# Kernel optimization log

Measured on AMD Instinct MI355X. Metric: run time of the kernel, lower is better.

Reference implementation:

```python
import jax, jax.numpy as jnp
from jax import lax
import numpy as np


def _conv(x, w):
    # x: [B,Cin,H,W], w: [Cout,Cin,kh,kw] -> [B,Cout,H,W], SAME padding
    return lax.conv_general_dilated(x, w, (1, 1), 'SAME')


def setup_inputs() -> dict:
    key = jax.random.key(0)
    ks = jax.random.split(key, 16)
    B, Hh, W = 8, 256, 256
    inputs = jax.random.normal(ks[0], (B, Hh, W), jnp.float32)
    H0 = jax.random.normal(ks[1], (B, Hh, W), jnp.float32)
    C0 = jax.random.normal(ks[2], (B, 2, Hh, W), jnp.float32)
    # learned scalars: c2 ~ U(0,1), sf ~ N(0, 0.01) shifted away from 0 (it is a divisor)
    c2 = jax.random.uniform(ks[3], (1,), jnp.float32, 0.0, 1.0)
    sf = 0.01 * jax.random.normal(ks[4], (1,), jnp.float32) + 0.02
    # RedNet (assumed small conv encoder-decoder): 1->32->64->32->1, 3x3 SAME, ReLU
    w1 = 0.1 * jax.random.normal(ks[5], (32, 1, 3, 3), jnp.float32)
    b1 = jnp.zeros((32,), jnp.float32)
    w2 = 0.1 * jax.random.normal(ks[6], (64, 32, 3, 3), jnp.float32)
    b2 = jnp.zeros((64,), jnp.float32)
    w3 = 0.1 * jax.random.normal(ks[7], (32, 64, 3, 3), jnp.float32)
    b3 = jnp.zeros((32,), jnp.float32)
    w4 = 0.1 * jax.random.normal(ks[8], (1, 32, 3, 3), jnp.float32)
    b4 = jnp.zeros((1,), jnp.float32)
    return dict(inputs=inputs, H0=H0, C0=C0, c2=c2, sf=sf,
                w1=w1, b1=b1, w2=w2, b2=b2, w3=w3, b3=b3, w4=w4, b4=b4)


def reference(inputs, H0, C0, c2, sf, w1, b1, w2, b2, w3, b3, w4, b4):
    # Fixed 5-point Laplacian stencil (non-trainable in the original module)
    lap_k = jnp.array([[0., 1., 0.], [1., -4., 1.], [0., 1., 0.]],
                      dtype=inputs.dtype)[None, None]  # [1,1,3,3]

    # torch chain: C' = permute/matmul(Wcc^T)/permute + wcu*U
    #   reduces exactly to: C'[:,0] = inputs, C'[:,1] = C_old[:,0]
    C_new = jnp.stack([inputs, C0[:, 0]], axis=1)  # [B,2,H,W]

    V = inputs - H0  # [B,H,W]

    # H = whc . C' = 2*C'[:,0] - C'[:,1] = 2*inputs - C_old[:,0]
    lap = _conv(inputs[:, None], lap_k)[:, 0]  # [B,H,W]
    H = 2.0 * inputs - C0[:, 0] + c2 * lap

    # RedNet on scaled residual V
    h = (V / sf)[:, None]  # [B,1,H,W]
    h = jax.nn.relu(_conv(h, w1) + b1[None, :, None, None])
    h = jax.nn.relu(_conv(h, w2) + b2[None, :, None, None])
    h = jax.nn.relu(_conv(h, w3) + b3[None, :, None, None])
    V_hat = (_conv(h, w4) + b4[None, :, None, None])[:, 0] * sf  # [B,H,W]

    outputs = H + V_hat
    return (outputs, H, C_new, V, V_hat)
```

## Files before the change

kernel.cpp:

```cpp
#include <hip/hip_runtime.h>

#define PLANE 65536
#define WIDTH 256
#define PADW 258
#define PADPLANE 66564

typedef __bf16 v8bf __attribute__((ext_vector_type(8)));
typedef float  v4f  __attribute__((ext_vector_type(4)));

typedef const __attribute__((address_space(1))) unsigned int* gas_ptr;
typedef __attribute__((address_space(3))) unsigned int* las_ptr;

__device__ __forceinline__ void gl_lds(const void* g, void* l) {
  __builtin_amdgcn_global_load_lds((gas_ptr)g, (las_ptr)l, 16, 0, 0);
}

__device__ __forceinline__ int swz(int c) {
  return (c & ~7) | ((c & 7) ^ ((c >> 3) & 7));
}

__device__ __forceinline__ unsigned int pack2(float a, float b) {
  __bf16 ba = (__bf16)a, bb = (__bf16)b;
  unsigned short sa = __builtin_bit_cast(unsigned short, ba);
  unsigned short sb = __builtin_bit_cast(unsigned short, bb);
  return (unsigned int)sa | ((unsigned int)sb << 16);
}

#define WT_N 37440
#define ZR_N (8 * 1028 * 64)
__global__ __launch_bounds__(256) void wz_k(
    const float* __restrict__ w1, const float* __restrict__ w2,
    const float* __restrict__ w3, const float* __restrict__ w4,
    float* __restrict__ w1t, __bf16* __restrict__ B2t,
    __bf16* __restrict__ B3t, float* __restrict__ w4t,
    __bf16* __restrict__ a1, __bf16* __restrict__ a2,
    __bf16* __restrict__ a3)
{
  int t = blockIdx.x * 256 + threadIdx.x;
  if (t < WT_N) {
    if (t < 288) {
      int tap = t >> 5, cout = t & 31;
      w1t[t] = w1[cout * 9 + tap];
    }
    int t2 = t - 288;
    if (t2 >= 0 && t2 < 18432) {
      int cout = t2 / 288, k = t2 % 288;
      int tap = k / 32, cin = k % 32;
      B2t[t2] = (__bf16)w2[cout * 288 + cin * 9 + tap];
    }
    int t3 = t - (288 + 18432);
    if (t3 >= 0 && t3 < 18432) {
      int cout = t3 / 576, k = t3 % 576;
      int tap = k / 64, cin = k % 64;
      B3t[t3] = (__bf16)w3[cout * 576 + cin * 9 + tap];
    }
    int t4 = t - (288 + 18432 + 18432);
    if (t4 >= 0 && t4 < 288) {
      int tap = t4 >> 5, cin = t4 & 31;
      w4t[t4] = w4[cin * 9 + tap];
    }
    return;
  }
  int idx = t - WT_N;
  if (idx >= ZR_N) return;
  unsigned int* p; int C2;
  const int R1 = 8 * 1028 * 16, R2 = 8 * 1028 * 32;
  if (idx < R1)           { p = (unsigned int*)a1; C2 = 16; }
  else if (idx < R1 + R2) { p = (unsigned int*)a2; C2 = 32; idx -= R1; }
  else                    { p = (unsigned int*)a3; C2 = 16; idx -= R1 + R2; }
  int ch = idx % C2;
  int pr = idx / C2;
  int b = pr / 1028, r = pr % 1028;
  int y, x;
  if      (r < 258) { y = 0;           x = r; }
  else if (r < 516) { y = 257;         x = r - 258; }
  else if (r < 772) { y = r - 516 + 1; x = 0; }
  else              { y = r - 772 + 1; x = 257; }
  p[((size_t)b * PADPLANE + y * PADW + x) * C2 + ch] = 0;
}

__global__ __launch_bounds__(256) void prepconv1_k(
    const float* __restrict__ inputs, const float* __restrict__ H0,
    const float* __restrict__ C0, const float* __restrict__ c2p,
    const float* __restrict__ sfp, const float* __restrict__ w1t,
    const float* __restrict__ b1, float* __restrict__ dout,
    __bf16* __restrict__ act1)
{
  const int x = threadIdx.x, y = blockIdx.x, b = blockIdx.y;
  const int p = b * PLANE + y * WIDTH + x;
  const float c2 = c2p[0], sf = sfp[0], rsf = 1.0f / sf;

  float iv[3][3], hv[3][3];
  #pragma unroll
  for (int dy = 0; dy < 3; dy++) {
    int yy = y + dy - 1;
    #pragma unroll
    for (int dx = 0; dx < 3; dx++) {
      int xx = x + dx - 1;
      bool ok = (yy >= 0 && yy < 256 && xx >= 0 && xx < 256);
      int pn = p + (dy - 1) * WIDTH + (dx - 1);
      iv[dy][dx] = ok ? inputs[pn] : 0.f;
      hv[dy][dx] = ok ? H0[pn]     : 0.f;
    }
  }
  const float in = iv[1][1], h0 = hv[1][1];
  const float c0a = C0[b * 131072 + y * WIDTH + x];
  float lap = iv[0][1] + iv[2][1] + iv[1][0] + iv[1][2] - 4.f * in;
  float Hv = 2.f * in - c0a + c2 * lap;
  float V  = in - h0;
  dout[524288 + p]  = Hv;
  dout[2097152 + p] = V;
  dout[1048576 + b * 131072 + y * WIDTH + x]         = in;
  dout[1048576 + b * 131072 + 65536 + y * WIDTH + x] = c0a;

  float acc[32];
  #pragma unroll
  for (int i = 0; i < 32; i++) acc[i] = b1[i];
  #pragma unroll
  for (int tap = 0; tap < 9; tap++) {
    float v = (iv[tap / 3][tap % 3] - hv[tap / 3][tap % 3]) * rsf;
    const float* wp = w1t + tap * 32;
    #pragma unroll
    for (int i = 0; i < 32; i++) acc[i] = fmaf(wp[i], v, acc[i]);
  }
  unsigned int u[16];
  #pragma unroll
  for (int j = 0; j < 16; j++)
    u[j] = pack2(fmaxf(acc[2*j], 0.f), fmaxf(acc[2*j+1], 0.f));
  size_t pa = ((size_t)b * PADPLANE + (y+1) * PADW + (x+1)) * 32;
  uint4* op = reinterpret_cast<uint4*>(act1 + pa);
  #pragma unroll
  for (int j = 0; j < 4; j++)
    op[j] = make_uint4(u[4*j], u[4*j+1], u[4*j+2], u[4*j+3]);
}

#define C2ROWB 8320
template<int ROWS>
__global__ __launch_bounds__(256, 2) void conv2_k(
    const __bf16* __restrict__ in, const __bf16* __restrict__ Bt,
    const float* __restrict__ bias, __bf16* __restrict__ out)
{
  const int lane = threadIdx.x & 63, wave = threadIdx.x >> 6;
  const int l15 = lane & 15, q = lane >> 4;
  const int y0 = blockIdx.x * ROWS, xt = blockIdx.y, b = blockIdx.z;
  const int x0 = xt * 128;
  __shared__ __align__(16) char smem[3 * C2ROWB];
  const __bf16* plane = in + (size_t)b * PADPLANE * 32;

  auto stage = [&](int pr, char* lrow) {
    const char* g = (const char*)(plane + ((size_t)pr * PADW + x0) * 32);
    const int base = wave * 130;
    #pragma unroll
    for (int j = 0; j < 2; j++) {
      int c = base + j * 64 + lane;
      gl_lds(g + (size_t)swz(c) * 16, lrow + (base + j * 64) * 16);
    }
    if (lane < 2) {
      int c = base + 128 + lane;
      gl_lds(g + (size_t)swz(c) * 16, lrow + (base + 128) * 16);
    }
  };

  v8bf breg[9][4];
  #pragma unroll
  for (int tap = 0; tap < 9; tap++)
    #pragma unroll
    for (int nt = 0; nt < 4; nt++)
      breg[tap][nt] = *(const v8bf*)(Bt + (size_t)(nt * 16 + l15) * 288
                                        + tap * 32 + q * 8);
  float bv[4];
  #pragma unroll
  for (int nt = 0; nt < 4; nt++) bv[nt] = bias[nt * 16 + l15];

  #pragma unroll
  for (int r = 0; r < 3; r++) stage(y0 + r, smem + r * C2ROWB);
  __syncthreads();

  for (int i = 0; i < ROWS; i++) {
    v4f acc[2][4];
    #pragma unroll
    for (int mt = 0; mt < 2; mt++)
      #pragma unroll
      for (int nt = 0; nt < 4; nt++)
        acc[mt][nt] = (v4f){bv[nt], bv[nt], bv[nt], bv[nt]};

    #pragma unroll
    for (int tap = 0; tap < 9; tap++) {
      const int dy = tap / 3, dx = tap % 3;
      const char* srow = smem + ((i + dy) % 3) * C2ROWB;
      v8bf af[2];
      #pragma unroll
      for (int mt = 0; mt < 2; mt++) {
        int P = wave * 32 + mt * 16 + l15 + dx;
        af[mt] = *(const v8bf*)(srow + (size_t)swz(P * 4 + q) * 16);
      }
      #pragma unroll
      for (int mt = 0; mt < 2; mt++)
        #pragma unroll
        for (int nt = 0; nt < 4; nt++)
          acc[mt][nt] = __builtin_amdgcn_mfma_f32_16x16x32_bf16(
              af[mt], breg[tap][nt], acc[mt][nt], 0, 0, 0);
    }
    {
      size_t rb = ((size_t)b * PADPLANE + (size_t)(y0 + i + 1) * PADW
                   + x0 + 1) * 64;
      #pragma unroll
      for (int mt = 0; mt < 2; mt++) {
        #pragma unroll
        for (int r = 0; r < 4; r++) {
          size_t pa = rb + (size_t)(wave * 32 + mt * 16 + q * 4 + r) * 64;
          #pragma unroll
          for (int nt = 0; nt < 4; nt++)
            out[pa + nt * 16 + l15] = (__bf16)fmaxf(acc[mt][nt][r], 0.f);
        }
      }
    }
    __syncthreads();
    if (i + 3 < ROWS + 2)
      stage(y0 + i + 3, smem + (i % 3) * C2ROWB);
    __syncthreads();
  }
}

#define C3ROWB 16640
template<int ROWS>
__global__ __launch_bounds__(256, 2) void conv3_k(
    const __bf16* __restrict__ in, const __bf16* __restrict__ Bt,
    const float* __restrict__ bias, __bf16* __restrict__ out)
{
  const int lane = threadIdx.x & 63, wave = threadIdx.x >> 6;
  const int l15 = lane & 15, q = lane >> 4;
  const int y0 = blockIdx.x * ROWS, xt = blockIdx.y, b = blockIdx.z;
  const int x0 = xt * 128;
  __shared__ __align__(16) char smem[4 * C3ROWB];
  const __bf16* plane = in + (size_t)b * PADPLANE * 64;

  auto stage = [&](int pr, char* lrow) {
    const char* g = (const char*)(plane + ((size_t)pr * PADW + x0) * 64);
    const int base = wave * 260;
    #pragma unroll
    for (int j = 0; j < 4; j++) {
      int c = base + j * 64 + lane;
      gl_lds(g + (size_t)swz(c) * 16, lrow + (base + j * 64) * 16);
    }
    if (lane < 4) {
      int c = base + 256 + lane;
      gl_lds(g + (size_t)swz(c) * 16, lrow + (base + 256) * 16);
    }
  };

  v8bf breg[9][2][2];
  #pragma unroll
  for (int tap = 0; tap < 9; tap++)
    #pragma unroll
    for (int kb = 0; kb < 2; kb++)
      #pragma unroll
      for (int nt = 0; nt < 2; nt++)
        breg[tap][kb][nt] = *(const v8bf*)(Bt + (size_t)(nt * 16 + l15) * 576
                                              + tap * 64 + kb * 32 + q * 8);
  float bv[2] = {bias[l15], bias[16 + l15]};

  #pragma unroll
  for (int r = 0; r < 4; r++) stage(y0 + r, smem + r * C3ROWB);
  __syncthreads();

  for (int ps = 0; ps < ROWS / 2; ps++) {
    v4f acc[2][2][2];
    #pragma unroll
    for (int rr = 0; rr < 2; rr++)
      #pragma unroll
      for (int mt = 0; mt < 2; mt++)
        #pragma unroll
        for (int nt = 0; nt < 2; nt++)
          acc[rr][mt][nt] = (v4f){bv[nt], bv[nt], bv[nt], bv[nt]};

    #pragma unroll
    for (int t = 0; t < 4; t++) {
      const char* srow = smem + ((2 * ps + t) & 3) * C3ROWB;
      #pragma unroll
      for (int dx = 0; dx < 3; dx++) {
        #pragma unroll
        for (int kb = 0; kb < 2; kb++) {
          v8bf af[2];
          #pragma unroll
          for (int mt = 0; mt < 2; mt++) {
            int P = wave * 32 + mt * 16 + l15 + dx;
            af[mt] = *(const v8bf*)(srow + (size_t)swz(P * 8 + kb * 4 + q) * 16);
          }
          #pragma unroll
          for (int mt = 0; mt < 2; mt++)
            #pragma unroll
            for (int nt = 0; nt < 2; nt++) {
              if (t <= 2)
                acc[0][mt][nt] = __builtin_amdgcn_mfma_f32_16x16x32_bf16(
                    af[mt], breg[t * 3 + dx][kb][nt], acc[0][mt][nt], 0, 0, 0);
              if (t >= 1)
                acc[1][mt][nt] = __builtin_amdgcn_mfma_f32_16x16x32_bf16(
                    af[mt], breg[(t - 1) * 3 + dx][kb][nt], acc[1][mt][nt],
                    0, 0, 0);
            }
        }
      }
    }
    {
      #pragma unroll
      for (int rr = 0; rr < 2; rr++) {
        size_t rb = ((size_t)b * PADPLANE
                     + (size_t)(y0 + 2 * ps + rr + 1) * PADW + x0 + 1) * 32;
        #pragma unroll
        for (int mt = 0; mt < 2; mt++) {
          #pragma unroll
          for (int r = 0; r < 4; r++) {
            size_t pa = rb + (size_t)(wave * 32 + mt * 16 + q * 4 + r) * 32;
            #pragma unroll
            for (int nt = 0; nt < 2; nt++)
              out[pa + nt * 16 + l15] = (__bf16)fmaxf(acc[rr][mt][nt][r], 0.f);
          }
        }
      }
    }
    __syncthreads();
    if (ps + 1 < ROWS / 2) {
      stage(y0 + 2 * ps + 4, smem + ((2 * ps) & 3) * C3ROWB);
      stage(y0 + 2 * ps + 5, smem + ((2 * ps + 1) & 3) * C3ROWB);
    }
    __syncthreads();
  }
}

__global__ __launch_bounds__(256) void conv4_k(
    const __bf16* __restrict__ act3, const float* __restrict__ w4t,
    const float* __restrict__ b4, const float* __restrict__ sfp,
    float* __restrict__ dout)
{
  const int x = threadIdx.x, y0 = blockIdx.x * 2, b = blockIdx.y;
  const float b4v = b4[0], sf = sfp[0];
  const uint4* base = (const uint4*)(act3 + (size_t)b * PADPLANE * 32);
  float acc0 = b4v, acc1 = b4v;

  #pragma unroll
  for (int t = 0; t < 4; t++) {
    const uint4* rp = base + ((size_t)(y0 + t) * PADW + x) * 4;
    uint4 L[12];
    #pragma unroll
    for (int j = 0; j < 12; j++) L[j] = rp[j];
    #pragma unroll
    for (int j = 0; j < 12; j++) {
      const int dx = j >> 2, c0 = (j & 3) * 8;
      unsigned int uu[4] = {L[j].x, L[j].y, L[j].z, L[j].w};
      float f[8];
      #pragma unroll
      for (int k = 0; k < 4; k++) {
        f[2*k]   = __builtin_bit_cast(float, uu[k] << 16);
        f[2*k+1] = __builtin_bit_cast(float, uu[k] & 0xFFFF0000u);
      }
      if (t <= 2) {
        const float* wp = w4t + (t * 3 + dx) * 32 + c0;
        #pragma unroll
        for (int k = 0; k < 8; k++) acc0 = fmaf(wp[k], f[k], acc0);
      }
      if (t >= 1) {
        const float* wp = w4t + ((t - 1) * 3 + dx) * 32 + c0;
        #pragma unroll
        for (int k = 0; k < 8; k++) acc1 = fmaf(wp[k], f[k], acc1);
      }
    }
  }
  size_t p0 = ((size_t)b << 16) + (size_t)y0 * WIDTH + x;
  float vh0 = acc0 * sf, vh1 = acc1 * sf;
  dout[p0]                   = dout[524288 + p0] + vh0;
  dout[2621440 + p0]         = vh0;
  dout[p0 + WIDTH]           = dout[524288 + p0 + WIDTH] + vh1;
  dout[2621440 + p0 + WIDTH] = vh1;
}

extern "C" void kernel_launch(void* const* d_in, const int* in_sizes, int n_in,
                              void* d_out, int out_size, void* d_ws, size_t ws_size,
                              hipStream_t stream) {
  const float* inputs = (const float*)d_in[0];
  const float* H0     = (const float*)d_in[1];
  const float* C0     = (const float*)d_in[2];
  const float* c2     = (const float*)d_in[3];
  const float* sf     = (const float*)d_in[4];
  const float* w1     = (const float*)d_in[5];
  const float* b1     = (const float*)d_in[6];
  const float* w2     = (const float*)d_in[7];
  const float* b2     = (const float*)d_in[8];
  const float* w3     = (const float*)d_in[9];
  const float* b3     = (const float*)d_in[10];
  const float* w4     = (const float*)d_in[11];
  const float* b4     = (const float*)d_in[12];
  float* out = (float*)d_out;
  float* ws  = (float*)d_ws;

  float*  w1t  = ws;
  float*  w4t  = ws + 288;
  __bf16* B2t  = (__bf16*)(ws + 576);
  __bf16* B3t  = (__bf16*)(ws + 9792);
  __bf16* act1 = (__bf16*)(ws + 19008);
  __bf16* act2 = act1 + (size_t)8 * PADPLANE * 32;
  __bf16* act3 = act2 + (size_t)8 * PADPLANE * 64;

  wz_k<<<2203, 256, 0, stream>>>(w1, w2, w3, w4, w1t, B2t, B3t, w4t,
                                 act1, act2, act3);
  prepconv1_k<<<dim3(256, 8), 256, 0, stream>>>(inputs, H0, C0, c2, sf,
                                                w1t, b1, out, act1);
  conv2_k<8><<<dim3(32, 2, 8), 256, 0, stream>>>(act1, B2t, b2, act2);
  conv3_k<8><<<dim3(32, 2, 8), 256, 0, stream>>>(act2, B3t, b3, act3);
  conv4_k<<<dim3(128, 8), 256, 0, stream>>>(act3, w4t, b4, sf, out);
}
```

Baseline: 170.6 us.

## Prefetch conv rows asynchronously with deeper LDS ring and retile conv3/conv4

Conv2 and conv3 now issue the global-to-LDS loads for upcoming rows at the top of each iteration, into a larger ring buffer (4 rows and 8 rows). They wait with partial vmcnt counts and a single barrier instead of two full __syncthreads, and raise wave priority around the MFMA section. This is meant to overlap staging with compute. Conv3 uses a 64-pixel-wide tile per block (doubling the grid) with one M tile per wave, and conv4 computes four output rows per thread instead of two to reuse loaded rows. The risks are correctness of the hand-tuned vmcnt counts and lower MFMA density per wave in conv3.

```diff
diff --git a/kernel.cpp b/kernel.cpp
--- a/kernel.cpp
+++ b/kernel.cpp
@@ -144,7 +144,7 @@
   const int l15 = lane & 15, q = lane >> 4;
   const int y0 = blockIdx.x * ROWS, xt = blockIdx.y, b = blockIdx.z;
   const int x0 = xt * 128;
-  __shared__ __align__(16) char smem[3 * C2ROWB];
+  __shared__ __align__(16) char smem[4 * C2ROWB];
   const __bf16* plane = in + (size_t)b * PADPLANE * 32;
 
   auto stage = [&](int pr, char* lrow) {
@@ -174,9 +174,14 @@
 
   #pragma unroll
   for (int r = 0; r < 3; r++) stage(y0 + r, smem + r * C2ROWB);
-  __syncthreads();
+  asm volatile("s_waitcnt vmcnt(0)" ::: "memory");
+  __builtin_amdgcn_s_barrier();
+  __builtin_amdgcn_sched_barrier(0);
 
   for (int i = 0; i < ROWS; i++) {
+    if (i + 3 < ROWS + 2)
+      stage(y0 + i + 3, smem + ((i + 3) & 3) * C2ROWB);
+
     v4f acc[2][4];
     #pragma unroll
     for (int mt = 0; mt < 2; mt++)
@@ -184,10 +189,11 @@
       for (int nt = 0; nt < 4; nt++)
         acc[mt][nt] = (v4f){bv[nt], bv[nt], bv[nt], bv[nt]};
 
+    __builtin_amdgcn_s_setprio(1);
     #pragma unroll
     for (int tap = 0; tap < 9; tap++) {
       const int dy = tap / 3, dx = tap % 3;
-      const char* srow = smem + ((i + dy) % 3) * C2ROWB;
+      const char* srow = smem + ((i + dy) & 3) * C2ROWB;
       v8bf af[2];
       #pragma unroll
       for (int mt = 0; mt < 2; mt++) {
@@ -201,6 +207,7 @@
           acc[mt][nt] = __builtin_amdgcn_mfma_f32_16x16x32_bf16(
               af[mt], breg[tap][nt], acc[mt][nt], 0, 0, 0);
     }
+    __builtin_amdgcn_s_setprio(0);
     {
       size_t rb = ((size_t)b * PADPLANE + (size_t)(y0 + i + 1) * PADW
                    + x0 + 1) * 64;
@@ -215,14 +222,13 @@
         }
       }
     }
-    __syncthreads();
-    if (i + 3 < ROWS + 2)
-      stage(y0 + i + 3, smem + (i % 3) * C2ROWB);
-    __syncthreads();
-  }
-}
-
-#define C3ROWB 16640
+    asm volatile("s_waitcnt vmcnt(24)" ::: "memory");
+    __builtin_amdgcn_s_barrier();
+    __builtin_amdgcn_sched_barrier(0);
+  }
+}
+
+#define C3ROWB 8448
 template<int ROWS>
 __global__ __launch_bounds__(256, 2) void conv3_k(
     const __bf16* __restrict__ in, const __bf16* __restrict__ Bt,
@@ -231,21 +237,21 @@
   const int lane = threadIdx.x & 63, wave = threadIdx.x >> 6;
   const int l15 = lane & 15, q = lane >> 4;
   const int y0 = blockIdx.x * ROWS, xt = blockIdx.y, b = blockIdx.z;
-  const int x0 = xt * 128;
-  __shared__ __align__(16) char smem[4 * C3ROWB];
+  const int x0 = xt * 64;
+  __shared__ __align__(16) char smem[8 * C3ROWB];
   const __bf16* plane = in + (size_t)b * PADPLANE * 64;
 
   auto stage = [&](int pr, char* lrow) {
     const char* g = (const char*)(plane + ((size_t)pr * PADW + x0) * 64);
-    const int base = wave * 260;
-    #pragma unroll
-    for (int j = 0; j < 4; j++) {
+    const int base = wave * 132;
+    #pragma unroll
+    for (int j = 0; j < 2; j++) {
       int c = base + j * 64 + lane;
       gl_lds(g + (size_t)swz(c) * 16, lrow + (base + j * 64) * 16);
     }
     if (lane < 4) {
-      int c = base + 256 + lane;
-      gl_lds(g + (size_t)swz(c) * 16, lrow + (base + 256) * 16);
+      int c = base + 128 + lane;
+      gl_lds(g + (size_t)swz(c) * 16, lrow + (base + 128) * 16);
     }
   };
 
@@ -262,69 +268,63 @@
 
   #pragma unroll
   for (int r = 0; r < 4; r++) stage(y0 + r, smem + r * C3ROWB);
-  __syncthreads();
+  asm volatile("s_waitcnt vmcnt(0)" ::: "memory");
+  __builtin_amdgcn_s_barrier();
+  __builtin_amdgcn_sched_barrier(0);
 
   for (int ps = 0; ps < ROWS / 2; ps++) {
-    v4f acc[2][2][2];
+    if (2 * ps + 4 < ROWS + 2)
+      stage(y0 + 2 * ps + 4, smem + ((2 * ps + 4) & 7) * C3ROWB);
+    if (2 * ps + 5 < ROWS + 2)
+      stage(y0 + 2 * ps + 5, smem + ((2 * ps + 5) & 7) * C3ROWB);
+
+    v4f acc[2][2];
     #pragma unroll
     for (int rr = 0; rr < 2; rr++)
       #pragma unroll
-      for (int mt = 0; mt < 2; mt++)
-        #pragma unroll
-        for (int nt = 0; nt < 2; nt++)
-          acc[rr][mt][nt] = (v4f){bv[nt], bv[nt], bv[nt], bv[nt]};
-
+      for (int nt = 0; nt < 2; nt++)
+        acc[rr][nt] = (v4f){bv[nt], bv[nt], bv[nt], bv[nt]};
+
+    __builtin_amdgcn_s_setprio(1);
     #pragma unroll
     for (int t = 0; t < 4; t++) {
-      const char* srow = smem + ((2 * ps + t) & 3) * C3ROWB;
+      const char* srow = smem + ((2 * ps + t) & 7) * C3ROWB;
       #pragma unroll
       for (int dx = 0; dx < 3; dx++) {
         #pragma unroll
         for (int kb = 0; kb < 2; kb++) {
-          v8bf af[2];
+          int P = wave * 16 + l15 + dx;
+          v8bf af = *(const v8bf*)(srow + (size_t)swz(P * 8 + kb * 4 + q) * 16);
           #pragma unroll
-          for (int mt = 0; mt < 2; mt++) {
-            int P = wave * 32 + mt * 16 + l15 + dx;
-            af[mt] = *(const v8bf*)(srow + (size_t)swz(P * 8 + kb * 4 + q) * 16);
+          for (int nt = 0; nt < 2; nt++) {
+            if (t <= 2)
+              acc[0][nt] = __builtin_amdgcn_mfma_f32_16x16x32_bf16(
+                  af, breg[t * 3 + dx][kb][nt], acc[0][nt], 0, 0, 0);
+            if (t >= 1)
+              acc[1][nt] = __builtin_amdgcn_mfma_f32_16x16x32_bf16(
+                  af, breg[(t - 1) * 3 + dx][kb][nt], acc[1][nt], 0, 0, 0);
           }
-          #pragma unroll
-          for (int mt = 0; mt < 2; mt++)
-            #pragma unroll
-            for (int nt = 0; nt < 2; nt++) {
-              if (t <= 2)
-                acc[0][mt][nt] = __builtin_amdgcn_mfma_f32_16x16x32_bf16(
-                    af[mt], breg[t * 3 + dx][kb][nt], acc[0][mt][nt], 0, 0, 0);
-              if (t >= 1)
-                acc[1][mt][nt] = __builtin_amdgcn_mfma_f32_16x16x32_bf16(
-                    af[mt], breg[(t - 1) * 3 + dx][kb][nt], acc[1][mt][nt],
-                    0, 0, 0);
-            }
         }
       }
     }
+    __builtin_amdgcn_s_setprio(0);
     {
       #pragma unroll
       for (int rr = 0; rr < 2; rr++) {
         size_t rb = ((size_t)b * PADPLANE
                      + (size_t)(y0 + 2 * ps + rr + 1) * PADW + x0 + 1) * 32;
         #pragma unroll
-        for (int mt = 0; mt < 2; mt++) {
+        for (int r = 0; r < 4; r++) {
+          size_t pa = rb + (size_t)(wave * 16 + q * 4 + r) * 32;
           #pragma unroll
-          for (int r = 0; r < 4; r++) {
-            size_t pa = rb + (size_t)(wave * 32 + mt * 16 + q * 4 + r) * 32;
-            #pragma unroll
-            for (int nt = 0; nt < 2; nt++)
-              out[pa + nt * 16 + l15] = (__bf16)fmaxf(acc[rr][mt][nt][r], 0.f);
-          }
+          for (int nt = 0; nt < 2; nt++)
+            out[pa + nt * 16 + l15] = (__bf16)fmaxf(acc[rr][nt][r], 0.f);
         }
       }
     }
-    __syncthreads();
-    if (ps + 1 < ROWS / 2) {
-      stage(y0 + 2 * ps + 4, smem + ((2 * ps) & 3) * C3ROWB);
-      stage(y0 + 2 * ps + 5, smem + ((2 * ps + 1) & 3) * C3ROWB);
-    }
-    __syncthreads();
+    asm volatile("s_waitcnt vmcnt(12)" ::: "memory");
+    __builtin_amdgcn_s_barrier();
+    __builtin_amdgcn_sched_barrier(0);
   }
 }
 
@@ -333,13 +333,13 @@
     const float* __restrict__ b4, const float* __restrict__ sfp,
     float* __restrict__ dout)
 {
-  const int x = threadIdx.x, y0 = blockIdx.x * 2, b = blockIdx.y;
+  const int x = threadIdx.x, y0 = blockIdx.x * 4, b = blockIdx.y;
   const float b4v = b4[0], sf = sfp[0];
   const uint4* base = (const uint4*)(act3 + (size_t)b * PADPLANE * 32);
-  float acc0 = b4v, acc1 = b4v;
-
-  #pragma unroll
-  for (int t = 0; t < 4; t++) {
+  float acc[4] = {b4v, b4v, b4v, b4v};
+
+  #pragma unroll
+  for (int t = 0; t < 6; t++) {
     const uint4* rp = base + ((size_t)(y0 + t) * PADW + x) * 4;
     uint4 L[12];
     #pragma unroll
@@ -354,24 +354,23 @@
         f[2*k]   = __builtin_bit_cast(float, uu[k] << 16);
         f[2*k+1] = __builtin_bit_cast(float, uu[k] & 0xFFFF0000u);
       }
-      if (t <= 2) {
-        const float* wp = w4t + (t * 3 + dx) * 32 + c0;
-        #pragma unroll
-        for (int k = 0; k < 8; k++) acc0 = fmaf(wp[k], f[k], acc0);
-      }
-      if (t >= 1) {
-        const float* wp = w4t + ((t - 1) * 3 + dx) * 32 + c0;
-        #pragma unroll
-        for (int k = 0; k < 8; k++) acc1 = fmaf(wp[k], f[k], acc1);
+      #pragma unroll
+      for (int r = 0; r < 4; r++) {
+        if (t - r >= 0 && t - r <= 2) {
+          const float* wp = w4t + ((t - r) * 3 + dx) * 32 + c0;
+          #pragma unroll
+          for (int k = 0; k < 8; k++) acc[r] = fmaf(wp[k], f[k], acc[r]);
+        }
       }
     }
   }
   size_t p0 = ((size_t)b << 16) + (size_t)y0 * WIDTH + x;
-  float vh0 = acc0 * sf, vh1 = acc1 * sf;
-  dout[p0]                   = dout[524288 + p0] + vh0;
-  dout[2621440 + p0]         = vh0;
-  dout[p0 + WIDTH]           = dout[524288 + p0 + WIDTH] + vh1;
-  dout[2621440 + p0 + WIDTH] = vh1;
+  #pragma unroll
+  for (int r = 0; r < 4; r++) {
+    float vh = acc[r] * sf;
+    dout[p0 + (size_t)r * WIDTH]           = dout[524288 + p0 + (size_t)r * WIDTH] + vh;
+    dout[2621440 + p0 + (size_t)r * WIDTH] = vh;
+  }
 }
 
 extern "C" void kernel_launch(void* const* d_in, const int* in_sizes, int n_in,
@@ -406,6 +405,6 @@
   prepconv1_k<<<dim3(256, 8), 256, 0, stream>>>(inputs, H0, C0, c2, sf,
                                                 w1t, b1, out, act1);
   conv2_k<8><<<dim3(32, 2, 8), 256, 0, stream>>>(act1, B2t, b2, act2);
-  conv3_k<8><<<dim3(32, 2, 8), 256, 0, stream>>>(act2, B3t, b3, act3);
-  conv4_k<<<dim3(128, 8), 256, 0, stream>>>(act3, w4t, b4, sf, out);
-}
+  conv3_k<8><<<dim3(32, 4, 8), 256, 0, stream>>>(act2, B3t, b3, act3);
+  conv4_k<<<dim3(64, 8), 256, 0, stream>>>(act3, w4t, b4, sf, out);
+}
```

New measurement: 246.6 us. 44.5% more time.
